# Performance work log

Measured on AMD Instinct MI355X. Metric: run time of the kernel, lower is better.

The kernel has to match this reference:

```python
import jax, jax.numpy as jnp
import numpy as np

B, D, L = 2, 1024, 4096   # batch, channels (= num_heads), seq len
FS = 4                    # filter_size
DEPTH = 11                # ceil(log2((L-1)/(FS-1)+1))
LN_EPS = 1e-5


def setup_inputs() -> dict:
    key = jax.random.key(0)
    ks = jax.random.split(key, 7)
    return {
        "x": jax.random.normal(ks[0], (B, D, L), jnp.float32),
        "h0": jax.random.normal(ks[1], (D, 1, FS), jnp.float32) * 0.2,
        "h1": jax.random.normal(ks[2], (D, 1, FS), jnp.float32) * 0.2,
        "w_mix": jax.random.normal(ks[3], (D, D), jnp.float32) / np.sqrt(D),
        "b_mix": jnp.zeros((D,), jnp.float32),
        "ln_gamma": jnp.ones((D,), jnp.float32),
        "ln_beta": jnp.zeros((D,), jnp.float32),
    }


def _dw_conv(a, h, dilation):
    # depthwise (groups = D) dilated conv1d, cross-correlation like torch
    return jax.lax.conv_general_dilated(
        a, h, window_strides=(1,), padding='VALID',
        rhs_dilation=(dilation,),
        dimension_numbers=('NCH', 'OIH', 'NCH'),
        feature_group_count=D)


def reference(x, h0, h1, w_mix, b_mix, ln_gamma, ln_beta):
    # --- multires conv tree ---
    a = x
    dilation = 1
    a_list, b_list = [], []
    for _ in range(DEPTH):
        pad = dilation * (FS - 1)
        ap = jnp.pad(a, ((0, 0), (0, 0), (pad, 0)))  # left causal pad
        b = _dw_conv(ap, h1, dilation)
        a = _dw_conv(ap, h0, dilation)
        a_list.append(a)
        b_list.append(b)
        dilation *= 2
    # --- gated combination across scales (deepest level first) ---
    a_rev = a_list[::-1]
    b_rev = b_list[::-1]
    y = jnp.zeros_like(x)
    gated = None
    for i in range(DEPTH):
        if i + 1 < DEPTH:
            gated = jax.nn.sigmoid(a_rev[i]) * b_rev[i + 1]
        # last iteration reuses the previous gated tensor (matches original)
        y = y + gated
    # --- 1x1 channel mix (Dropout1d is identity in eval) + residual ---
    mixed = jnp.einsum('oc,bcl->bol', w_mix, y) + b_mix[None, :, None]
    z = mixed + x
    # --- LayerNorm over channel dim ---
    mu = jnp.mean(z, axis=1, keepdims=True)
    var = jnp.mean(jnp.square(z - mu), axis=1, keepdims=True)
    out = (z - mu) * jax.lax.rsqrt(var + LN_EPS)
    out = out * ln_gamma[None, :, None] + ln_beta[None, :, None]
    return out
```

## Files before the change

kernel.cpp:

```cpp
#include <hip/hip_runtime.h>
#include <hip/hip_bf16.h>
#include <hip/hip_fp16.h>

#define NB 2
#define ND 1024
#define NL 4096
#define NFS 4
#define NDEPTH 11
#define LN_EPS 1e-5f

#define BM 128
#define BN 128
#define BK 32
#define NKI (ND / BK)
#define ASZ (BM * BK)

#define CPAD 3072
#define CBUF (CPAD + NL)

typedef __bf16 bf16x8 __attribute__((ext_vector_type(8)));
typedef float f32x4 __attribute__((ext_vector_type(4)));
typedef _Float16 half8 __attribute__((ext_vector_type(8)));

__device__ __forceinline__ unsigned short f2bf(float f) {
    __hip_bfloat16 h = __float2bfloat16(f);
    unsigned short u;
    __builtin_memcpy(&u, &h, 2);
    return u;
}

__device__ __forceinline__ float bf2f(unsigned short u) {
    unsigned int ui = (unsigned int)u << 16;
    float f;
    __builtin_memcpy(&f, &ui, 4);
    return f;
}

__device__ __forceinline__ unsigned int pack2bf(float lo, float hi) {
    return (unsigned int)f2bf(lo) | ((unsigned int)f2bf(hi) << 16);
}

__device__ __forceinline__ void llds16(const void* g, void* l) {
    __builtin_amdgcn_global_load_lds(
        (const __attribute__((address_space(1))) unsigned int*)g,
        (__attribute__((address_space(3))) unsigned int*)l, 16, 0, 0);
}

__device__ __forceinline__ half8 ldx8(const float* p) {
    const float4 v0 = *reinterpret_cast<const float4*>(p);
    const float4 v1 = *reinterpret_cast<const float4*>(p + 4);
    half8 r;
    r[0] = (_Float16)v0.x; r[1] = (_Float16)v0.y;
    r[2] = (_Float16)v0.z; r[3] = (_Float16)v0.w;
    r[4] = (_Float16)v1.x; r[5] = (_Float16)v1.y;
    r[6] = (_Float16)v1.z; r[7] = (_Float16)v1.w;
    return r;
}

__device__ __forceinline__ half8 ldx8z(const float* xrow, int off) {
    half8 v = ldx8(xrow + (off >= 0 ? off : 0));
    return (off >= 0) ? v : (half8)0;
}

__global__ __launch_bounds__(256) void wconv_kernel(const float* __restrict__ w,
                                                    unsigned short* __restrict__ wbf) {
    const int idx8 = (blockIdx.x * 256 + threadIdx.x) * 8;
    const float4 v0 = *reinterpret_cast<const float4*>(w + idx8);
    const float4 v1 = *reinterpret_cast<const float4*>(w + idx8 + 4);
    uint4 o;
    o.x = pack2bf(v0.x, v0.y);
    o.y = pack2bf(v0.z, v0.w);
    o.z = pack2bf(v1.x, v1.y);
    o.w = pack2bf(v1.z, v1.w);
    *reinterpret_cast<uint4*>(wbf + idx8) = o;
}

__global__ __launch_bounds__(512) void conv_cascade_kernel(const float* __restrict__ x,
                                                           const float* __restrict__ h0,
                                                           const float* __restrict__ h1,
                                                           unsigned short* __restrict__ ybf) {
    __shared__ _Float16 a_sh[2][CBUF];
    const int row = blockIdx.x;
    const int d = row & (ND - 1);
    const int t = threadIdx.x;

    if (t < CPAD / 8) {
        *reinterpret_cast<half8*>(&a_sh[0][t * 8]) = (half8)0;
        *reinterpret_cast<half8*>(&a_sh[1][t * 8]) = (half8)0;
    }

    const float* xrow = x + (size_t)row * NL;

    _Float16 h0c[NFS], h1c[NFS];
#pragma unroll
    for (int k = 0; k < NFS; ++k) {
        h0c[k] = (_Float16)h0[d * NFS + k];
        h1c[k] = (_Float16)h1[d * NFS + k];
    }

    const int l8 = t * 8;
    const int A = CPAD + l8;

    const half8 X0 = ldx8z(xrow, l8 - 32);
    const half8 X1 = ldx8z(xrow, l8 - 24);
    const half8 X2 = ldx8z(xrow, l8 - 16);
    const half8 X3 = ldx8z(xrow, l8 - 8);
    const half8 C  = ldx8(xrow + l8);

    const __half2 nlog2e = __float2half2_rn(-1.44269504f);
    const __half2 one2 = __float2half2_rn(1.f);
    const __half2 two2 = __float2half2_rn(2.f);
    __half2 yacc2[4];
#pragma unroll
    for (int p = 0; p < 4; ++p) yacc2[p] = __float2half2_rn(0.f);

#define SH1(L, R) __builtin_shufflevector(L, R, 7, 8, 9, 10, 11, 12, 13, 14)
#define SH2(L, R) __builtin_shufflevector(L, R, 6, 7, 8, 9, 10, 11, 12, 13)
#define SH3(L, R) __builtin_shufflevector(L, R, 5, 6, 7, 8, 9, 10, 11, 12)
#define SH4(L, R) __builtin_shufflevector(L, R, 4, 5, 6, 7, 8, 9, 10, 11)
#define SH6(L, R) __builtin_shufflevector(L, R, 2, 3, 4, 5, 6, 7, 8, 9)
#define CONV_D1(L, R, hc) ((R)*hc[3] + SH1(L, R) * hc[2] + SH2(L, R) * hc[1] + SH3(L, R) * hc[0])
#define CONV_D2(L, R, hc) ((R)*hc[3] + SH2(L, R) * hc[2] + SH4(L, R) * hc[1] + SH6(L, R) * hc[0])

#define GATE(av, bv, SC2)                                           \
    {                                                               \
        __half2 ap_[4], bp_[4];                                     \
        __builtin_memcpy(ap_, &(av), 16);                           \
        __builtin_memcpy(bp_, &(bv), 16);                           \
        _Pragma("unroll") for (int p = 0; p < 4; ++p) {             \
            const __half2 e = h2exp2(__hmul2(ap_[p], nlog2e));      \
            const __half2 s = h2rcp(__hadd2(e, one2));              \
            const __half2 g = __hmul2(__hmul2(s, bp_[p]), SC2);     \
            yacc2[p] = __hadd2(g, yacc2[p]);                        \
        }                                                           \
    }

    const half8 a0_1 = CONV_D1(X0, X1, h0c);
    const half8 a0_2 = CONV_D1(X1, X2, h0c);
    const half8 a0_3 = CONV_D1(X2, X3, h0c);
    const half8 a0_4 = CONV_D1(X3, C, h0c);
    const half8 b0 = CONV_D1(X3, C, h1c);

    const half8 a1_2 = CONV_D2(a0_1, a0_2, h0c);
    const half8 a1_3 = CONV_D2(a0_2, a0_3, h0c);
    const half8 a1_4 = CONV_D2(a0_3, a0_4, h0c);
    const half8 b1 = CONV_D2(a0_3, a0_4, h1c);
    GATE(a1_4, b0, two2)

    const half8 s4 = SH4(a1_3, a1_4);
    const half8 s12 = SH4(a1_2, a1_3);
    const half8 a2 = a1_4 * h0c[3] + s4 * h0c[2] + a1_3 * h0c[1] + s12 * h0c[0];
    const half8 b2 = a1_4 * h1c[3] + s4 * h1c[2] + a1_3 * h1c[1] + s12 * h1c[0];
    GATE(a2, b1, one2)

    half8 cur = a2;
    half8 bprev = b2;
    _Float16* rbp = &a_sh[0][0];
    _Float16* wbp = &a_sh[1][0];
    *reinterpret_cast<half8*>(&rbp[A]) = cur;
    __syncthreads();

    half8 an, bn;
#define CMATH(a1v, a2v, a3v)                                              \
    an = cur * h0c[3] + (a1v)*h0c[2] + (a2v)*h0c[1] + (a3v)*h0c[0];       \
    bn = cur * h1c[3] + (a1v)*h1c[2] + (a2v)*h1c[1] + (a3v)*h1c[0];
#define CFIN()                                                            \
    {                                                                     \
        *reinterpret_cast<half8*>(&wbp[A]) = an;                          \
        cur = an;                                                         \
        bprev = bn;                                                       \
        _Float16* tmpp = rbp; rbp = wbp; wbp = tmpp;                      \
    }

    int dil = 8;
#pragma unroll 1
    for (int lev = 3; lev <= 9; ++lev) {
        const half8 a1v = *reinterpret_cast<const half8*>(&rbp[A - dil]);
        const half8 a2v = *reinterpret_cast<const half8*>(&rbp[A - 2 * dil]);
        const half8 a3v = *reinterpret_cast<const half8*>(&rbp[A - 3 * dil]);
        CMATH(a1v, a2v, a3v)
        GATE(an, bprev, one2)
        CFIN()
        dil <<= 1;
        __syncthreads();
    }

    {
        const half8 a1v = *reinterpret_cast<const half8*>(&rbp[A - 1024]);
        const half8 a2v = *reinterpret_cast<const half8*>(&rbp[A - 2048]);
        const half8 a3v = *reinterpret_cast<const half8*>(&rbp[A - 3072]);
        an = cur * h0c[3] + a1v * h0c[2] + a2v * h0c[1] + a3v * h0c[0];
        GATE(an, bprev, one2)
    }
#undef CMATH
#undef GATE
#undef CFIN
#undef CONV_D1
#undef CONV_D2
#undef SH1
#undef SH2
#undef SH3
#undef SH4
#undef SH6

    const float2 f0 = __half22float2(yacc2[0]);
    const float2 f1 = __half22float2(yacc2[1]);
    const float2 f2 = __half22float2(yacc2[2]);
    const float2 f3 = __half22float2(yacc2[3]);
    uint4 o;
    o.x = pack2bf(f0.x, f0.y);
    o.y = pack2bf(f1.x, f1.y);
    o.z = pack2bf(f2.x, f2.y);
    o.w = pack2bf(f3.x, f3.y);
    *reinterpret_cast<uint4*>(ybf + (size_t)row * NL + t * 8) = o;
}

__global__ __launch_bounds__(256) void transpose_kernel(const unsigned short* __restrict__ ybf,
                                                        unsigned short* __restrict__ yT) {
    __shared__ unsigned short tile[64][66];
    const int l0 = blockIdx.x * 64;
    const int c0 = blockIdx.y * 64;
    const int b = blockIdx.z;
    const int t = threadIdx.x;
    const int li = t & 63, cg = t >> 6;
#pragma unroll
    for (int k = 0; k < 16; ++k) {
        const int ci = cg * 16 + k;
        tile[ci][li] = ybf[(size_t)(b * ND + c0 + ci) * NL + l0 + li];
    }
    __syncthreads();
    const int ci2 = t & 63, lg = t >> 6;
#pragma unroll
    for (int k = 0; k < 16; ++k) {
        const int li2 = lg * 16 + k;
        yT[((size_t)b * NL + l0 + li2) * ND + c0 + ci2] = tile[ci2][li2];
    }
}

__global__ __launch_bounds__(256) void gemm_kernel(const unsigned short* __restrict__ wbf,
                                                   const unsigned short* __restrict__ yT,
                                                   const float* __restrict__ bmix,
                                                   unsigned short* __restrict__ mixed) {
    __shared__ unsigned short As[3][BM][BK];
    __shared__ unsigned short Bs[3][BN][BK];

    const int orig = blockIdx.x;
    const int wgid = (orig & 7) * 64 + (orig >> 3);
    const int b = wgid & 1;
    const int m0 = ((wgid >> 1) & 7) * BM;
    const int n0 = (wgid >> 4) * BN;

    const int t = threadIdx.x;
    const int lane = t & 63, wid = t >> 6;
    const int wr = wid >> 1, wc = wid & 1;
    const int fr = lane & 15;
    const int fk = (lane >> 4) * 8;

    const int srow = wid * 32 + (lane >> 2);
    const int sk = (lane & 3) * 8;
    const unsigned short* Ag = wbf + (size_t)(m0 + srow) * ND + sk;
    const unsigned short* Bg = yT + ((size_t)b * NL + n0 + srow) * ND + sk;
    unsigned short* A0 = &As[0][0][0];
    unsigned short* B0 = &Bs[0][0][0];
    unsigned short* AsW = A0 + wid * 32 * BK;
    unsigned short* BsW = B0 + wid * 32 * BK;

#define STAGE(bo, kt)                           \
    llds16(Ag + (kt), AsW + (bo));              \
    llds16(Ag + (kt) + 16 * ND, AsW + (bo) + 16 * BK); \
    llds16(Bg + (kt), BsW + (bo));              \
    llds16(Bg + (kt) + 16 * ND, BsW + (bo) + 16 * BK);

    f32x4 acc[4][4];
#pragma unroll
    for (int mi = 0; mi < 4; ++mi)
#pragma unroll
        for (int ni = 0; ni < 4; ++ni)
            acc[mi][ni] = (f32x4){0.f, 0.f, 0.f, 0.f};

    STAGE(0, 0)
    STAGE(ASZ, BK)

    int bc = 0;
    int bs = 2;
#pragma unroll 1
    for (int ki = 0; ki < NKI; ++ki) {
        if (ki + 1 < NKI) {
            asm volatile("s_waitcnt vmcnt(4)" ::: "memory");
        } else {
            asm volatile("s_waitcnt vmcnt(0)" ::: "memory");
        }
        __builtin_amdgcn_s_barrier();
        __builtin_amdgcn_sched_barrier(0);

        if (ki + 2 < NKI) {
            const int bo = bs * ASZ;
            const int kt = (ki + 2) * BK;
            STAGE(bo, kt)
        }

        const int bco = bc * ASZ;
        bf16x8 af[4], bv[4];
#pragma unroll
        for (int mi = 0; mi < 4; ++mi)
            af[mi] = *reinterpret_cast<const bf16x8*>(A0 + bco + (wr * 64 + mi * 16 + fr) * BK + fk);
#pragma unroll
        for (int ni = 0; ni < 4; ++ni)
            bv[ni] = *reinterpret_cast<const bf16x8*>(B0 + bco + (wc * 64 + ni * 16 + fr) * BK + fk);
#pragma unroll
        for (int mi = 0; mi < 4; ++mi)
#pragma unroll
            for (int ni = 0; ni < 4; ++ni)
                acc[mi][ni] = __builtin_amdgcn_mfma_f32_16x16x32_bf16(af[mi], bv[ni],
                                                                      acc[mi][ni], 0, 0, 0);
        bc = (bc == 2) ? 0 : bc + 1;
        bs = (bs == 2) ? 0 : bs + 1;
    }
#undef STAGE

    const size_t bbase = (size_t)b * ND * NL;
#pragma unroll
    for (int mi = 0; mi < 4; ++mi) {
#pragma unroll
        for (int r = 0; r < 4; ++r) {
            const int o = m0 + wr * 64 + mi * 16 + (lane >> 4) * 4 + r;
            const float bm = bmix[o];
            const size_t rowbase = bbase + (size_t)o * NL;
#pragma unroll
            for (int ni = 0; ni < 4; ++ni) {
                const int l = n0 + wc * 64 + ni * 16 + fr;
                mixed[rowbase + l] = f2bf(acc[mi][ni][r] + bm);
            }
        }
    }
}

__global__ __launch_bounds__(1024) void ln_kernel(const unsigned short* __restrict__ mixed,
                                                  const float* __restrict__ x,
                                                  const float* __restrict__ gamma,
                                                  const float* __restrict__ beta,
                                                  float* __restrict__ out) {
    __shared__ float gsh[ND], bsh[ND];
    __shared__ float sred[32][33], qred[32][33];
    __shared__ float mu_s[32], rs_s[32];

    const int t = threadIdx.x;
    gsh[t] = gamma[t];
    bsh[t] = beta[t];

    const int b = blockIdx.y;
    const int l0 = blockIdx.x * 32;
    const int tl = t & 31, tg = t >> 5;
    const size_t base = (size_t)b * ND * NL + l0 + tl;

    float zv[32];
    float s = 0.f, q = 0.f;
#pragma unroll
    for (int j = 0; j < 32; ++j) {
        const size_t idx = base + (size_t)(tg + j * 32) * NL;
        const float v = bf2f(mixed[idx]) + x[idx];
        zv[j] = v;
        s += v;
        q += v * v;
    }

    sred[tg][tl] = s;
    qred[tg][tl] = q;
    __syncthreads();
    if (tg == 0) {
        float S = 0.f, Q = 0.f;
#pragma unroll
        for (int g = 0; g < 32; ++g) {
            S += sred[g][tl];
            Q += qred[g][tl];
        }
        const float mu = S * (1.f / ND);
        const float var = Q * (1.f / ND) - mu * mu;
        mu_s[tl] = mu;
        rs_s[tl] = rsqrtf(var + LN_EPS);
    }
    __syncthreads();
    const float mu = mu_s[tl], rs = rs_s[tl];
#pragma unroll
    for (int j = 0; j < 32; ++j) {
        const int c = tg + j * 32;
        out[base + (size_t)c * NL] = (zv[j] - mu) * rs * gsh[c] + bsh[c];
    }
}

extern "C" void kernel_launch(void* const* d_in, const int* in_sizes, int n_in,
                              void* d_out, int out_size, void* d_ws, size_t ws_size,
                              hipStream_t stream) {
    (void)in_sizes; (void)n_in; (void)out_size; (void)ws_size;
    const float* x = (const float*)d_in[0];
    const float* h0 = (const float*)d_in[1];
    const float* h1 = (const float*)d_in[2];
    const float* wmix = (const float*)d_in[3];
    const float* bmix = (const float*)d_in[4];
    const float* gamma = (const float*)d_in[5];
    const float* beta = (const float*)d_in[6];
    float* out = (float*)d_out;

    char* ws = (char*)d_ws;
    unsigned short* ybf = (unsigned short*)(ws);
    unsigned short* yT = (unsigned short*)(ws + (size_t)16 * 1024 * 1024);
    unsigned short* wbf = (unsigned short*)(ws + (size_t)32 * 1024 * 1024);
    unsigned short* mixed = (unsigned short*)(ws + (size_t)34 * 1024 * 1024);

    wconv_kernel<<<dim3(ND * ND / (256 * 8)), 256, 0, stream>>>(wmix, wbf);
    conv_cascade_kernel<<<dim3(NB * ND), 512, 0, stream>>>(x, h0, h1, ybf);
    transpose_kernel<<<dim3(NL / 64, ND / 64, NB), 256, 0, stream>>>(ybf, yT);
    gemm_kernel<<<dim3(512), 256, 0, stream>>>(wbf, yT, bmix, mixed);
    ln_kernel<<<dim3(NL / 32, NB), 1024, 0, stream>>>(mixed, x, gamma, beta, out);
}
```

Baseline: 93.26 us.

## Fuse conv tree level pairs and vectorize transpose with swizzled LDS

The conv tree loop now computes two dilation levels per barrier. It recomputes the intermediate level's needed taps from nine shared-memory reads of the previous buffer, which removes roughly half the __syncthreads and LDS round-trips in exchange for extra FMAs. The transpose kernel switches to 16-byte vector loads and stores with an XOR-swizzled LDS tile to avoid bank conflicts, replacing scalar 2-byte global accesses. Risks include higher register pressure in the conv kernel and scalar gathers from LDS on the transpose read side.

Result: slower. 96.51 us (+3.5%).

```diff
diff --git a/kernel.cpp b/kernel.cpp
--- a/kernel.cpp
+++ b/kernel.cpp
@@ -21,6 +21,7 @@
 typedef __bf16 bf16x8 __attribute__((ext_vector_type(8)));
 typedef float f32x4 __attribute__((ext_vector_type(4)));
 typedef _Float16 half8 __attribute__((ext_vector_type(8)));
+typedef unsigned short ushort8 __attribute__((ext_vector_type(8)));
 
 __device__ __forceinline__ unsigned short f2bf(float f) {
     __hip_bfloat16 h = __float2bfloat16(f);
@@ -160,28 +161,48 @@
     *reinterpret_cast<half8*>(&rbp[A]) = cur;
     __syncthreads();
 
-    half8 an, bn;
-#define CMATH(a1v, a2v, a3v)                                              \
-    an = cur * h0c[3] + (a1v)*h0c[2] + (a2v)*h0c[1] + (a3v)*h0c[0];       \
-    bn = cur * h1c[3] + (a1v)*h1c[2] + (a2v)*h1c[1] + (a3v)*h1c[0];
-#define CFIN()                                                            \
-    {                                                                     \
-        *reinterpret_cast<half8*>(&wbp[A]) = an;                          \
-        cur = an;                                                         \
-        bprev = bn;                                                       \
-        _Float16* tmpp = rbp; rbp = wbp; wbp = tmpp;                      \
-    }
-
-    int dil = 8;
-#pragma unroll 1
-    for (int lev = 3; lev <= 9; ++lev) {
-        const half8 a1v = *reinterpret_cast<const half8*>(&rbp[A - dil]);
-        const half8 a2v = *reinterpret_cast<const half8*>(&rbp[A - 2 * dil]);
-        const half8 a3v = *reinterpret_cast<const half8*>(&rbp[A - 3 * dil]);
-        CMATH(a1v, a2v, a3v)
+#define PAIR(DD)                                                                     \
+    {                                                                                \
+        const half8 t1 = *reinterpret_cast<const half8*>(&rbp[A - (DD)]);            \
+        const half8 t2 = *reinterpret_cast<const half8*>(&rbp[A - 2 * (DD)]);        \
+        const half8 t3 = *reinterpret_cast<const half8*>(&rbp[A - 3 * (DD)]);        \
+        const half8 t4 = *reinterpret_cast<const half8*>(&rbp[A - 4 * (DD)]);        \
+        const half8 t5 = *reinterpret_cast<const half8*>(&rbp[A - 5 * (DD)]);        \
+        const half8 t6 = *reinterpret_cast<const half8*>(&rbp[A - 6 * (DD)]);        \
+        const half8 t7 = *reinterpret_cast<const half8*>(&rbp[A - 7 * (DD)]);        \
+        const half8 t8 = *reinterpret_cast<const half8*>(&rbp[A - 8 * (DD)]);        \
+        const half8 t9 = *reinterpret_cast<const half8*>(&rbp[A - 9 * (DD)]);        \
+        const half8 aL0 = cur * h0c[3] + t1 * h0c[2] + t2 * h0c[1] + t3 * h0c[0];    \
+        const half8 aL2 = t2 * h0c[3] + t3 * h0c[2] + t4 * h0c[1] + t5 * h0c[0];     \
+        const half8 aL4 = t4 * h0c[3] + t5 * h0c[2] + t6 * h0c[1] + t7 * h0c[0];     \
+        const half8 aL6 = t6 * h0c[3] + t7 * h0c[2] + t8 * h0c[1] + t9 * h0c[0];     \
+        const half8 bL0 = cur * h1c[3] + t1 * h1c[2] + t2 * h1c[1] + t3 * h1c[0];    \
+        GATE(aL0, bprev, one2)                                                       \
+        const half8 aN = aL0 * h0c[3] + aL2 * h0c[2] + aL4 * h0c[1] + aL6 * h0c[0];  \
+        const half8 bN = aL0 * h1c[3] + aL2 * h1c[2] + aL4 * h1c[1] + aL6 * h1c[0];  \
+        GATE(aN, bL0, one2)                                                          \
+        *reinterpret_cast<half8*>(&wbp[A]) = aN;                                     \
+        cur = aN;                                                                    \
+        bprev = bN;                                                                  \
+        { _Float16* tmpp = rbp; rbp = wbp; wbp = tmpp; }                             \
+        __syncthreads();                                                             \
+    }
+
+    PAIR(8)
+    PAIR(32)
+    PAIR(128)
+
+    {
+        const half8 a1v = *reinterpret_cast<const half8*>(&rbp[A - 512]);
+        const half8 a2v = *reinterpret_cast<const half8*>(&rbp[A - 1024]);
+        const half8 a3v = *reinterpret_cast<const half8*>(&rbp[A - 1536]);
+        const half8 an = cur * h0c[3] + a1v * h0c[2] + a2v * h0c[1] + a3v * h0c[0];
+        const half8 bn = cur * h1c[3] + a1v * h1c[2] + a2v * h1c[1] + a3v * h1c[0];
         GATE(an, bprev, one2)
-        CFIN()
-        dil <<= 1;
+        *reinterpret_cast<half8*>(&wbp[A]) = an;
+        cur = an;
+        bprev = bn;
+        { _Float16* tmpp = rbp; rbp = wbp; wbp = tmpp; }
         __syncthreads();
     }
 
@@ -189,12 +210,12 @@
         const half8 a1v = *reinterpret_cast<const half8*>(&rbp[A - 1024]);
         const half8 a2v = *reinterpret_cast<const half8*>(&rbp[A - 2048]);
         const half8 a3v = *reinterpret_cast<const half8*>(&rbp[A - 3072]);
-        an = cur * h0c[3] + a1v * h0c[2] + a2v * h0c[1] + a3v * h0c[0];
+        const half8 an = cur * h0c[3] + a1v * h0c[2] + a2v * h0c[1] + a3v * h0c[0];
         GATE(an, bprev, one2)
     }
+#undef PAIR
 #undef CMATH
 #undef GATE
-#undef CFIN
 #undef CONV_D1
 #undef CONV_D2
 #undef SH1
@@ -217,23 +238,37 @@
 
 __global__ __launch_bounds__(256) void transpose_kernel(const unsigned short* __restrict__ ybf,
                                                         unsigned short* __restrict__ yT) {
-    __shared__ unsigned short tile[64][66];
+    __shared__ unsigned short tile[64 * 64];
     const int l0 = blockIdx.x * 64;
     const int c0 = blockIdx.y * 64;
     const int b = blockIdx.z;
     const int t = threadIdx.x;
-    const int li = t & 63, cg = t >> 6;
-#pragma unroll
-    for (int k = 0; k < 16; ++k) {
-        const int ci = cg * 16 + k;
-        tile[ci][li] = ybf[(size_t)(b * ND + c0 + ci) * NL + l0 + li];
+
+    const int li8 = (t & 7) * 8;
+    const int ci_ = t >> 3;
+#pragma unroll
+    for (int p = 0; p < 2; ++p) {
+        const int ci = ci_ + p * 32;
+        const ushort8 v = *reinterpret_cast<const ushort8*>(
+            ybf + (size_t)(b * ND + c0 + ci) * NL + l0 + li8);
+        const int blk = ((li8 >> 3) ^ ((ci >> 3) ^ ci)) & 7;
+        *reinterpret_cast<ushort8*>(&tile[ci * 64 + blk * 8]) = v;
     }
     __syncthreads();
-    const int ci2 = t & 63, lg = t >> 6;
-#pragma unroll
-    for (int k = 0; k < 16; ++k) {
-        const int li2 = lg * 16 + k;
-        yT[((size_t)b * NL + l0 + li2) * ND + c0 + ci2] = tile[ci2][li2];
+
+    const int li_ = t >> 3;
+    const int cv8 = (t & 7) * 8;
+#pragma unroll
+    for (int p = 0; p < 2; ++p) {
+        const int li = li_ + p * 32;
+        ushort8 o;
+#pragma unroll
+        for (int j = 0; j < 8; ++j) {
+            const int r = cv8 + j;
+            const int blk = ((li >> 3) ^ ((r >> 3) ^ r)) & 7;
+            o[j] = tile[r * 64 + blk * 8 + (li & 7)];
+        }
+        *reinterpret_cast<ushort8*>(yT + ((size_t)b * NL + l0 + li) * ND + c0 + cv8) = o;
     }
 }
 
```
